# Kernel optimization log

Measured on AMD Instinct MI355X. Metric: run time of the kernel, lower is better.

Reference implementation:

```python
import jax, jax.numpy as jnp
import numpy as np
import math

B, C, T0, Q0 = 2, 48, 250, 65
H = 192; KS = 4; HS = 1; NH = 4; E = 8; F = 65; DV = 12; HID2 = 384
EPS = 1e-5


def ln_clamp(x, g, b, axes, eps=EPS):
    # LayerNormalization4D / 4DCF: std = sqrt(clamp(var, eps))
    mu = x.mean(axis=axes, keepdims=True)
    var = x.var(axis=axes, keepdims=True)
    return (x - mu) / jnp.sqrt(jnp.maximum(var, eps)) * g + b


def torch_ln(x, g, b, eps=EPS):
    # torch.nn.LayerNorm over last dim: sqrt(var + eps)
    mu = x.mean(axis=-1, keepdims=True)
    var = x.var(axis=-1, keepdims=True)
    return (x - mu) / jnp.sqrt(var + eps) * g + b


def mha(x, in_w, in_b, out_w, out_b, nh):
    # torch.nn.MultiheadAttention, batch_first, self-attention
    N, L, Cm = x.shape
    qkv = x @ in_w.T + in_b
    q, k, v = jnp.split(qkv, 3, axis=-1)
    dh = Cm // nh
    hd = lambda t: t.reshape(N, L, nh, dh).transpose(0, 2, 1, 3)
    q, k, v = hd(q), hd(k), hd(v)
    att = jax.nn.softmax(jnp.einsum('nhld,nhmd->nhlm', q, k) / jnp.sqrt(jnp.float32(dh)), axis=-1)
    o = jnp.einsum('nhlm,nhmd->nhld', att, v).transpose(0, 2, 1, 3).reshape(N, L, Cm)
    return o @ out_w.T + out_b


def lstm_dir(x, wi, wh, bi, bh, reverse=False):
    # x: [N, L, D]; torch gate order i,f,g,o
    Hd = wh.shape[1]
    xs = jnp.swapaxes(x, 0, 1)
    if reverse:
        xs = xs[::-1]
    pre = jnp.einsum('lnd,gd->lng', xs, wi) + bi + bh  # [L,N,4H]

    def step(carry, p):
        hprev, cprev = carry
        gates = p + hprev @ wh.T
        i, f, g, o = jnp.split(gates, 4, axis=-1)
        c = jax.nn.sigmoid(f) * cprev + jax.nn.sigmoid(i) * jnp.tanh(g)
        hnew = jax.nn.sigmoid(o) * jnp.tanh(c)
        return (hnew, c), hnew

    h0 = jnp.zeros((x.shape[0], Hd), x.dtype)
    _, ys = jax.lax.scan(step, (h0, h0), pre)
    if reverse:
        ys = ys[::-1]
    return jnp.swapaxes(ys, 0, 1)


def bilstm(x, wif, whf, bif, bhf, wib, whb, bib, bhb):
    return jnp.concatenate([lstm_dir(x, wif, whf, bif, bhf, False),
                            lstm_dir(x, wib, whb, bib, bhb, True)], axis=-1)


def unfold1d(x, ks, hs):
    # x: [N, C, Q] -> [N, L, C*ks], channel-major like F.unfold
    N, Cc, Qq = x.shape
    L = (Qq - ks) // hs + 1
    cols = jnp.stack([x[:, :, k:k + (L - 1) * hs + 1:hs] for k in range(ks)], axis=-1)  # [N,C,L,ks]
    return cols.transpose(0, 2, 1, 3).reshape(N, L, Cc * ks)


def conv_transpose1d(x, w, b, stride):
    # x: [N, Cin, L], w: [Cin, Cout, ks] (torch ConvTranspose1d layout); overlap-add
    N, Ci, L = x.shape
    ks = w.shape[2]
    out_len = (L - 1) * stride + ks
    y = jnp.einsum('nil,iok->nolk', x, w)
    out = jnp.zeros((N, w.shape[1], out_len), x.dtype)
    for k in range(ks):
        out = out.at[:, :, k:k + (L - 1) * stride + 1:stride].add(y[..., k])
    return out + b[:, None]


def _forward(x, af_in_w, af_in_b, af_out_w, af_out_b, naf_g, naf_b, at_in_w, at_in_b, at_out_w, at_out_b, nat_g, nat_b, intra_ng, intra_nb, inter_ng, inter_nb, intra_wif, intra_whf, intra_bif, intra_bhf, intra_wib, intra_whb, intra_bib, intra_bhb, inter_wif, inter_whf, inter_bif, inter_bhf, inter_wib, inter_whb, inter_bib, inter_bhb, il_w, il_b, itl_w, itl_b, qw, qb, qa, qg, qbt, kw, kb, ka, kg, kbt, vw, vb, va, vg, vbt, pw, pb, pa, pg, pbt, fin_w, fin_b, fdw_w, fdw_b, fout_w, fout_b):
    Bb, Cc, old_T, old_Q = x.shape
    T = math.ceil((old_T - KS) / HS) * HS + KS
    Qd = math.ceil((old_Q - KS) / HS) * HS + KS
    x = jnp.pad(x, ((0, 0), (0, 0), (0, T - old_T), (0, Qd - old_Q)))
    input_ = x

    # ---- intra (frequency) path ----
    z = ln_clamp(input_, intra_ng[None, :, None, None], intra_nb[None, :, None, None], (1,))
    seq = z.transpose(0, 2, 3, 1).reshape(Bb * T, Qd, Cc)  # [B*T, Q, C]
    att = mha(seq, af_in_w, af_in_b, af_out_w, af_out_b, NH)
    seq = torch_ln(att + seq, naf_g, naf_b)
    u = unfold1d(seq.transpose(0, 2, 1), KS, HS)
    r = bilstm(u, intra_wif, intra_whf, intra_bif, intra_bhf, intra_wib, intra_whb, intra_bib, intra_bhb)
    r = conv_transpose1d(r.transpose(0, 2, 1), il_w, il_b, HS)  # [B*T, C, Qd]
    intra = r.reshape(Bb, T, Cc, Qd).transpose(0, 2, 1, 3) + input_
    input_ = intra

    # ---- inter (time) path ----
    z = ln_clamp(input_, inter_ng[None, :, None, None], inter_nb[None, :, None, None], (1,))
    seq = z.transpose(0, 3, 2, 1).reshape(Bb * Qd, T, Cc)  # [B*Q, T, C]
    att = mha(seq, at_in_w, at_in_b, at_out_w, at_out_b, NH)
    seq = torch_ln(att + seq, nat_g, nat_b)
    u = unfold1d(seq.transpose(0, 2, 1), KS, HS)
    r = bilstm(u, inter_wif, inter_whf, inter_bif, inter_bhf, inter_wib, inter_whb, inter_bib, inter_bhb)
    r = conv_transpose1d(r.transpose(0, 2, 1), itl_w, itl_b, HS)  # [B*Qd, C, T]
    inter = r.reshape(Bb, Qd, Cc, T).transpose(0, 2, 3, 1) + input_
    inter = inter[:, :, :old_T, :old_Q]

    # ---- custom per-head conv attention ----
    bt = inter  # [B, C, t, f]

    def head_proj(w, bias, a, g, beta):
        y = jnp.einsum('bctf,hec->hbetf', bt, w) + bias[:, None, :, None, None]
        y = jnp.where(y >= 0, y, a[:, None, None, None, None] * y)  # PReLU per head
        return ln_clamp(y, g[:, None, :, None, :], beta[:, None, :, None, :], (2, 4))

    Qh = head_proj(qw, qb, qa, qg, qbt)  # [h,B,E,t,f]
    Kh = head_proj(kw, kb, ka, kg, kbt)
    Vh = head_proj(vw, vb, va, vg, vbt)  # [h,B,dv,t,f]
    h_, _, E_, t_, f_ = Qh.shape
    dv = Vh.shape[2]
    Qf = Qh.transpose(0, 1, 3, 2, 4).reshape(h_, Bb, t_, E_ * f_)
    Kf = Kh.transpose(0, 1, 3, 2, 4).reshape(h_, Bb, t_, E_ * f_)
    Vf = Vh.transpose(0, 1, 3, 2, 4).reshape(h_, Bb, t_, dv * f_)
    attm = jax.nn.softmax(jnp.einsum('hbtd,hbsd->hbts', Qf, Kf) / jnp.sqrt(jnp.float32(E_ * f_)), axis=-1)
    Vo = jnp.einsum('hbts,hbsd->hbtd', attm, Vf).reshape(h_, Bb, t_, dv, f_)
    Vo = Vo.transpose(1, 0, 3, 2, 4).reshape(Bb, h_ * dv, t_, f_)  # head-major channel concat
    pj = jnp.einsum('bctf,oc->botf', Vo, pw) + pb[None, :, None, None]
    pj = jnp.where(pj >= 0, pj, pa * pj)
    pj = ln_clamp(pj, pg[None, :, None, :], pbt[None, :, None, :], (1, 3))
    out = pj + inter

    # ---- gated-dconv FFN ----
    pi = jnp.einsum('bctf,oc->botf', out, fin_w) + fin_b[None, :, None, None]
    dwc = jax.lax.conv_general_dilated(pi, fdw_w, (1, 1), ((1, 1), (1, 1)),
                                       dimension_numbers=('NCHW', 'OIHW', 'NCHW'),
                                       feature_group_count=fdw_w.shape[0]) + fdw_b[None, :, None, None]
    x1, x2 = jnp.split(dwc, 2, axis=1)
    ffn = jnp.einsum('bctf,oc->botf', jax.nn.gelu(x1, approximate=False) * x2, fout_w) + fout_b[None, :, None, None]
    return ffn + out


def setup_inputs() -> dict:
    key = jax.random.key(0)
    cnt = [0]

    def rn(shape, s=0.05):
        cnt[0] += 1
        return jax.random.normal(jax.random.fold_in(key, cnt[0]), shape, dtype=jnp.float32) * s

    z = lambda *s: jnp.zeros(s, jnp.float32)
    o = lambda *s: jnp.ones(s, jnp.float32)
    d = {}
    d['x'] = rn((B, C, T0, Q0), 1.0)
    for p in ['af', 'at']:
        d[p + '_in_w'] = rn((3 * C, C)); d[p + '_in_b'] = z(3 * C)
        d[p + '_out_w'] = rn((C, C)); d[p + '_out_b'] = z(C)
    d['naf_g'] = o(C); d['naf_b'] = z(C); d['nat_g'] = o(C); d['nat_b'] = z(C)
    d['intra_ng'] = o(C); d['intra_nb'] = z(C); d['inter_ng'] = o(C); d['inter_nb'] = z(C)
    for p in ['intra', 'inter']:
        for s in ['f', 'b']:
            d[p + '_wi' + s] = rn((4 * H, C * KS)); d[p + '_wh' + s] = rn((4 * H, H))
            d[p + '_bi' + s] = z(4 * H); d[p + '_bh' + s] = z(4 * H)
    d['il_w'] = rn((2 * H, C, KS)); d['il_b'] = z(C)
    d['itl_w'] = rn((2 * H, C, KS)); d['itl_b'] = z(C)
    for p, dim in [('q', E), ('k', E), ('v', DV)]:
        d[p + 'w'] = rn((NH, dim, C)); d[p + 'b'] = z(NH, dim)
        d[p + 'a'] = 0.25 * o(NH); d[p + 'g'] = o(NH, dim, F); d[p + 'bt'] = z(NH, dim, F)
    d['pw'] = rn((C, C)); d['pb'] = z(C); d['pa'] = 0.25 * o(1); d['pg'] = o(C, F); d['pbt'] = z(C, F)
    d['fin_w'] = rn((HID2, C)); d['fin_b'] = z(HID2)
    d['fdw_w'] = rn((HID2, 1, 3, 3)); d['fdw_b'] = z(HID2)
    d['fout_w'] = rn((C, HID2 // 2)); d['fout_b'] = z(C)
    return d


def reference(x, af_in_w, af_in_b, af_out_w, af_out_b, naf_g, naf_b, at_in_w, at_in_b, at_out_w, at_out_b, nat_g, nat_b, intra_ng, intra_nb, inter_ng, inter_nb, intra_wif, intra_whf, intra_bif, intra_bhf, intra_wib, intra_whb, intra_bib, intra_bhb, inter_wif, inter_whf, inter_bif, inter_bhf, inter_wib, inter_whb, inter_bib, inter_bhb, il_w, il_b, itl_w, itl_b, qw, qb, qa, qg, qbt, kw, kb, ka, kg, kbt, vw, vb, va, vg, vbt, pw, pb, pa, pg, pbt, fin_w, fin_b, fdw_w, fdw_b, fout_w, fout_b):
    return _forward(x, af_in_w, af_in_b, af_out_w, af_out_b, naf_g, naf_b, at_in_w, at_in_b, at_out_w, at_out_b, nat_g, nat_b, intra_ng, intra_nb, inter_ng, inter_nb, intra_wif, intra_whf, intra_bif, intra_bhf, intra_wib, intra_whb, intra_bib, intra_bhb, inter_wif, inter_whf, inter_bif, inter_bhf, inter_wib, inter_whb, inter_bib, inter_bhb, il_w, il_b, itl_w, itl_b, qw, qb, qa, qg, qbt, kw, kb, ka, kg, kbt, vw, vb, va, vg, vbt, pw, pb, pa, pg, pbt, fin_w, fin_b, fdw_w, fdw_b, fout_w, fout_b)
```

## Files before the change

### kernel.cpp

```cpp
#include <hip/hip_runtime.h>
#include <math.h>

#define EPSV 1e-5f

typedef _Float16 v2h __attribute__((ext_vector_type(2)));

__device__ __forceinline__ float sigf(float x){ return 1.0f/(1.0f+__expf(-x)); }
__device__ __forceinline__ float tanhf_(float x){
  float c = fminf(fmaxf(x,-10.f),10.f);
  float e = __expf(2.0f*c);
  return (e-1.0f)/(e+1.0f);
}

__device__ __forceinline__ void ldsbar(){
  asm volatile("s_waitcnt lgkmcnt(0)\n\ts_barrier" ::: "memory");
}

__device__ __forceinline__ float dot2u(unsigned int a, unsigned int b, float c){
#if __has_builtin(__builtin_amdgcn_fdot2)
  v2h av = __builtin_bit_cast(v2h, a);
  v2h bv = __builtin_bit_cast(v2h, b);
  return __builtin_amdgcn_fdot2(av, bv, c, false);
#else
  v2h av = __builtin_bit_cast(v2h, a);
  v2h bv = __builtin_bit_cast(v2h, b);
  return c + (float)av.x*(float)bv.x + (float)av.y*(float)bv.y;
#endif
}

__global__ void k_ln_chan(const float* __restrict__ src, float* __restrict__ dst,
                          const float* __restrict__ g, const float* __restrict__ bb, int mode){
  int i = blockIdx.x*blockDim.x + threadIdx.x;
  const int total = 2*250*65;
  if (i >= total) return;
  int q = i % 65; int t = (i/65) % 250; int b = i/(65*250);
  const float* p = src + (size_t)b*48*250*65 + (size_t)t*65 + q;
  float s=0.f, ss=0.f;
  for (int c=0;c<48;c++){ float v = p[(size_t)c*250*65]; s+=v; ss+=v*v; }
  float mu = s*(1.0f/48.0f);
  float var = ss*(1.0f/48.0f) - mu*mu;
  float rs = rsqrtf(fmaxf(var, EPSV));
  float* d = (mode==0) ? dst + ((size_t)(b*250+t)*65 + q)*48
                       : dst + ((size_t)(b*65+q)*250 + t)*48;
  for (int c=0;c<48;c++){ float v = p[(size_t)c*250*65]; d[c] = (v-mu)*rs*g[c] + bb[c]; }
}

__global__ void k_qkv(const float* __restrict__ seq, const float* __restrict__ w,
                      const float* __restrict__ bias, float* __restrict__ qkv, int NL){
  int i = blockIdx.x*blockDim.x + threadIdx.x;
  if (i >= NL*144) return;
  int j = i % 144; int nl = i / 144;
  const float* srow = seq + (size_t)nl*48;
  const float* wrow = w + j*48;
  float acc = bias[j];
  for (int c=0;c<48;c++) acc += srow[c]*wrow[c];
  qkv[i] = acc;
}

__global__ void k_mha(const float* __restrict__ qkv, float* __restrict__ att, int N, int L){
  __shared__ float shq[250*12];
  __shared__ float shk[250*12];
  __shared__ float shv[250*12];
  int n = blockIdx.x, h = blockIdx.y;
  const float* base = qkv + (size_t)n*L*144 + h*12;
  for (int i = threadIdx.x; i < L*12; i += blockDim.x){
    int l = i/12, d = i%12;
    shq[i] = base[(size_t)l*144 + d];
    shk[i] = base[(size_t)l*144 + 48 + d];
    shv[i] = base[(size_t)l*144 + 96 + d];
  }
  __syncthreads();
  const float scale = 0.28867513459481287f;
  for (int r = threadIdx.x; r < L; r += blockDim.x){
    float m = -1e30f, den = 0.0f, o[12];
    for (int d=0; d<12; d++) o[d]=0.0f;
    const float* qr = shq + r*12;
    for (int j=0; j<L; j++){
      const float* kr = shk + j*12;
      float s = 0.f;
      for (int d=0; d<12; d++) s += qr[d]*kr[d];
      s *= scale;
      if (s > m){
        float corr = __expf(m - s);
        den *= corr;
        for (int d=0; d<12; d++) o[d] *= corr;
        m = s;
      }
      float e = __expf(s - m);
      den += e;
      const float* vr = shv + j*12;
      for (int d=0; d<12; d++) o[d] += e*vr[d];
    }
    float inv = 1.0f/den;
    float* outp = att + ((size_t)n*L + r)*48 + h*12;
    for (int d=0; d<12; d++) outp[d] = o[d]*inv;
  }
}

__global__ void k_projres(const float* __restrict__ att, const float* __restrict__ seq,
                          const float* __restrict__ w, const float* __restrict__ bias,
                          float* __restrict__ dst, int NL){
  int i = blockIdx.x*blockDim.x + threadIdx.x;
  if (i >= NL*48) return;
  int o = i % 48; int nl = i/48;
  const float* ar = att + (size_t)nl*48;
  const float* wr = w + o*48;
  float acc = bias[o] + seq[i];
  for (int c=0;c<48;c++) acc += ar[c]*wr[c];
  dst[i] = acc;
}

__global__ void k_rowln(float* __restrict__ buf, const float* __restrict__ g,
                        const float* __restrict__ bb, int NL){
  int nl = blockIdx.x*blockDim.x + threadIdx.x;
  if (nl >= NL) return;
  float* p = buf + (size_t)nl*48;
  float s=0.f, ss=0.f;
  for (int c=0;c<48;c++){ float v=p[c]; s+=v; ss+=v*v; }
  float mu = s*(1.0f/48.0f);
  float var = ss*(1.0f/48.0f) - mu*mu;
  float rs = rsqrtf(var + EPSV);
  for (int c=0;c<48;c++) p[c] = (p[c]-mu)*rs*g[c] + bb[c];
}

__global__ void k_prep(const float* __restrict__ s0, const float* __restrict__ s1,
                       const float* __restrict__ s2, const float* __restrict__ s3,
                       const float* __restrict__ s4, const float* __restrict__ s5,
                       const float* __restrict__ s6, const float* __restrict__ s7,
                       const float* __restrict__ c0, const float* __restrict__ c1,
                       unsigned int* __restrict__ wpk, unsigned int* __restrict__ wtp){
  int i = blockIdx.x*blockDim.x + threadIdx.x;
  if (i < 589824){
    int seg = i/73728, off = i - seg*73728;
    const float* w = (seg==0)?s0:(seg==1)?s1:(seg==2)?s2:(seg==3)?s3:(seg==4)?s4:(seg==5)?s5:(seg==6)?s6:s7;
    int g = off % 768, d2 = off / 768;
    v2h v; v.x = (_Float16)w[g*192 + 2*d2]; v.y = (_Float16)w[g*192 + 2*d2 + 1];
    wpk[(size_t)seg*73728 + (size_t)d2*768 + g] = __builtin_bit_cast(unsigned int, v);
  } else if (i < 589824 + 2*36864){
    int j = i - 589824;
    int seg = j/36864, off = j - seg*36864;
    const float* w = seg ? c1 : c0;
    int c = off % 48; int ii2 = (off/48) % 192; int k = off/(48*192);
    v2h v;
    v.x = (_Float16)w[(2*ii2)*192 + c*4 + k];
    v.y = (_Float16)w[(2*ii2+1)*192 + c*4 + k];
    wtp[(size_t)seg*36864 + off] = __builtin_bit_cast(unsigned int, v);
  }
}

__global__ __launch_bounds__(256) void k_pregates(
    const float* __restrict__ seq2, const unsigned int* __restrict__ wi,
    const float* __restrict__ bi, const float* __restrict__ bh,
    _Float16* __restrict__ pre, int L2, int SL){
  __shared__ unsigned int ut[96*16];
  int n = blockIdx.y;
  int l0 = blockIdx.x*16;
  int t = threadIdx.x;
  for (int idx=t; idx<1536; idx+=256){
    int l = idx & 15, d2 = idx >> 4;
    int li = l0 + l;
    int c = d2 >> 1, k0 = (d2 & 1)*2;
    float u0=0.f, u1=0.f;
    if (li < L2){
      const float* p = seq2 + ((size_t)n*SL + li)*48;
      u0 = p[k0*48 + c];
      u1 = p[(k0+1)*48 + c];
    }
    v2h v; v.x=(_Float16)u0; v.y=(_Float16)u1;
    ut[d2*16 + l] = __builtin_bit_cast(unsigned int, v);
  }
  __syncthreads();
  float acc[3][16];
  float b0 = bi[t] + bh[t];
  float b1 = bi[t+256] + bh[t+256];
  float b2 = bi[t+512] + bh[t+512];
  #pragma unroll
  for (int l=0;l<16;l++){ acc[0][l]=b0; acc[1][l]=b1; acc[2][l]=b2; }
  #pragma unroll 4
  for (int d2=0; d2<96; d2++){
    unsigned int w0 = wi[(size_t)d2*768 + t];
    unsigned int w1 = wi[(size_t)d2*768 + t + 256];
    unsigned int w2 = wi[(size_t)d2*768 + t + 512];
    const uint4* u4 = (const uint4*)(ut + d2*16);
    #pragma unroll
    for (int l4=0; l4<4; l4++){
      uint4 uu = u4[l4];
      acc[0][l4*4+0] = dot2u(uu.x, w0, acc[0][l4*4+0]);
      acc[0][l4*4+1] = dot2u(uu.y, w0, acc[0][l4*4+1]);
      acc[0][l4*4+2] = dot2u(uu.z, w0, acc[0][l4*4+2]);
      acc[0][l4*4+3] = dot2u(uu.w, w0, acc[0][l4*4+3]);
      acc[1][l4*4+0] = dot2u(uu.x, w1, acc[1][l4*4+0]);
      acc[1][l4*4+1] = dot2u(uu.y, w1, acc[1][l4*4+1]);
      acc[1][l4*4+2] = dot2u(uu.z, w1, acc[1][l4*4+2]);
      acc[1][l4*4+3] = dot2u(uu.w, w1, acc[1][l4*4+3]);
      acc[2][l4*4+0] = dot2u(uu.x, w2, acc[2][l4*4+0]);
      acc[2][l4*4+1] = dot2u(uu.y, w2, acc[2][l4*4+1]);
      acc[2][l4*4+2] = dot2u(uu.z, w2, acc[2][l4*4+2]);
      acc[2][l4*4+3] = dot2u(uu.w, w2, acc[2][l4*4+3]);
    }
  }
  #pragma unroll
  for (int l=0;l<16;l++){
    int li = l0 + l;
    if (li < L2){
      _Float16* pr = pre + ((size_t)n*L2 + li)*768;
      pr[t]       = (_Float16)acc[0][l];
      pr[t+256]   = (_Float16)acc[1][l];
      pr[t+512]   = (_Float16)acc[2][l];
    }
  }
}

template<int G>
__global__ __launch_bounds__(1024) void k_lstm6(
    const _Float16* __restrict__ pre, unsigned int* __restrict__ rT2,
    const unsigned int* __restrict__ wh_f, const unsigned int* __restrict__ wh_b,
    int N, int L2){
  __shared__ unsigned int hh2[96*G];
  __shared__ float gpart[4*G*768];
  _Float16* hh2h = (_Float16*)hh2;
  int t = threadIdx.x;
  int q = t >> 8, tt = t & 255;
  int dir = blockIdx.y;
  int n0 = blockIdx.x*G;
  const unsigned int* wh = dir ? wh_b : wh_f;
  unsigned int wq[24][3];
  #pragma unroll
  for (int i=0;i<24;i++){
    const unsigned int* wr = wh + (size_t)(q*24+i)*768 + tt;
    wq[i][0] = wr[0]; wq[i][1] = wr[256]; wq[i][2] = wr[512];
  }
  const _Float16* prd = pre + (size_t)dir*(size_t)N*L2*768;
  float cst = 0.f;
  int as = t/192, aj = t - as*192;
  bool actv = (t < 192*G);
  const unsigned short* pbase = (const unsigned short*)prd;
  if (actv) pbase = (const unsigned short*)(prd + ((size_t)(n0+as)*L2)*768) + aj;
  for (int idx=t; idx<96*G; idx+=1024) hh2[idx]=0u;
  __syncthreads();

  unsigned short c0=0,c1=0,c2=0,c3=0;
  {
    int l0 = dir ? (L2-1) : 0;
    if (actv){
      const unsigned short* pp = pbase + (size_t)l0*768;
      c0 = pp[0]; c1 = pp[192]; c2 = pp[384]; c3 = pp[576];
    }
  }

  for (int step=0; step<L2; step++){
    int l = dir ? (L2-1-step) : step;
    int stepn = (step+1 < L2) ? (step+1) : step;
    int ln = dir ? (L2-1-stepn) : stepn;
    unsigned short pn0=0,pn1=0,pn2=0,pn3=0;
    if (actv){
      const unsigned short* pp = pbase + (size_t)ln*768;
      pn0 = pp[0]; pn1 = pp[192]; pn2 = pp[384]; pn3 = pp[576];
    }

    float acc0[G], acc1[G], acc2[G];
    #pragma unroll
    for (int s=0;s<G;s++){ acc0[s]=0.f; acc1[s]=0.f; acc2[s]=0.f; }
    #pragma unroll
    for (int i=0;i<24;i++){
      unsigned int hhv[G];
      if (G==4){
        uint4 hv = ((const uint4*)hh2)[q*24+i];
        hhv[0]=hv.x; hhv[1]=hv.y; hhv[2]=hv.z; hhv[3]=hv.w;
      } else if (G==2){
        uint2 hv = ((const uint2*)hh2)[q*24+i];
        hhv[0]=hv.x; hhv[1]=hv.y;
      } else {
        hhv[0] = hh2[q*24+i];
      }
      unsigned int w0 = wq[i][0], w1 = wq[i][1], w2 = wq[i][2];
      #pragma unroll
      for (int s=0;s<G;s++){
        acc0[s] = dot2u(hhv[s], w0, acc0[s]);
        acc1[s] = dot2u(hhv[s], w1, acc1[s]);
        acc2[s] = dot2u(hhv[s], w2, acc2[s]);
      }
    }
    #pragma unroll
    for (int s=0;s<G;s++){
      gpart[(q*G+s)*768 + tt]       = acc0[s];
      gpart[(q*G+s)*768 + tt + 256] = acc1[s];
      gpart[(q*G+s)*768 + tt + 512] = acc2[s];
    }
    ldsbar();

    if (actv){
      float gi = (float)__builtin_bit_cast(_Float16, c0);
      float gf = (float)__builtin_bit_cast(_Float16, c1);
      float gg = (float)__builtin_bit_cast(_Float16, c2);
      float go = (float)__builtin_bit_cast(_Float16, c3);
      #pragma unroll
      for (int qq=0; qq<4; qq++){
        const float* gp = gpart + (qq*G+as)*768;
        gi += gp[aj]; gf += gp[aj+192]; gg += gp[aj+384]; go += gp[aj+576];
      }
      float ig = sigf(gi), fg = sigf(gf), g2 = tanhf_(gg), og = sigf(go);
      cst = fg*cst + ig*g2;
      float hn = og*tanhf_(cst);
      hh2h[((aj>>1)*G + as)*2 + (aj&1)] = (_Float16)hn;
    }
    ldsbar();

    if (t < 96*G){
      int s = t/96, ii2 = t - s*96;
      unsigned int v = hh2[ii2*G + s];
      rT2[((size_t)(n0+s)*192 + dir*96 + ii2)*L2 + l] = v;
    }
    c0 = pn0; c1 = pn1; c2 = pn2; c3 = pn3;
  }
}

__global__ __launch_bounds__(256) void k_convt4(
    const unsigned int* __restrict__ rT2, const unsigned int* __restrict__ wtp,
    const float* __restrict__ bias, const float* __restrict__ resid,
    float* __restrict__ dst, int L2, int OL, int mode){
  int n = blockIdx.y;
  int pos = blockIdx.x*64 + (threadIdx.x & 63);
  int cq = __builtin_amdgcn_readfirstlane((int)(threadIdx.x >> 6));
  float acc[12];
  #pragma unroll
  for (int c=0;c<12;c++) acc[c]=0.f;
  const unsigned int* rbase = rT2 + (size_t)n*192*L2;
  for (int k=0;k<4;k++){
    int l = pos - k;
    bool v = (l>=0) && (l<L2);
    int lc = v ? l : 0;
    const unsigned int* wk = wtp + (size_t)k*192*48 + cq*12;
    #pragma unroll 4
    for (int ii2=0; ii2<192; ii2++){
      unsigned int rp = v ? rbase[(size_t)ii2*L2 + lc] : 0u;
      const unsigned int* wrow = wk + ii2*48;
      #pragma unroll
      for (int c=0;c<12;c++) acc[c] = dot2u(rp, wrow[c], acc[c]);
    }
  }
  if (pos < OL){
    for (int c12=0;c12<12;c12++){
      int c = cq*12 + c12;
      size_t oidx;
      if (mode==0){ int b=n/250, t=n%250; oidx = (((size_t)b*48+c)*250+t)*65+pos; }
      else        { int b=n/65,  qq=n%65; oidx = (((size_t)b*48+c)*250+pos)*65+qq; }
      dst[oidx] = acc[c12] + bias[c] + resid[oidx];
    }
  }
}

__global__ __launch_bounds__(256) void k_hproj(
    const float* __restrict__ bt, const float* __restrict__ w,
    const float* __restrict__ bias, const float* __restrict__ alpha,
    const float* __restrict__ g, const float* __restrict__ beta,
    float* __restrict__ dst, int dim, int kt_mode){
  __shared__ float ybuf[780];
  __shared__ float r1[256];
  __shared__ float r2[256];
  int bx = blockIdx.x;
  int h = bx/500; int rem = bx - h*500; int b = rem/250; int t = rem - b*250;
  int ny = dim*65;
  int tid = threadIdx.x;
  const float* bbase = bt + (size_t)b*48*250*65 + (size_t)t*65;
  float al = alpha[h];
  float s=0.f, ss=0.f;
  for (int kidx=tid; kidx<ny; kidx+=256){
    int e = kidx/65, f = kidx - e*65;
    const float* wr = w + (h*dim+e)*48;
    float acc = bias[h*dim+e];
    for (int c=0;c<48;c++) acc += bbase[(size_t)c*250*65 + f]*wr[c];
    if (acc < 0.f) acc *= al;
    ybuf[kidx] = acc; s += acc; ss += acc*acc;
  }
  r1[tid]=s; r2[tid]=ss; __syncthreads();
  for (int st=128; st>0; st>>=1){
    if (tid<st){ r1[tid]+=r1[tid+st]; r2[tid]+=r2[tid+st]; }
    __syncthreads();
  }
  float mu = r1[0]/(float)ny, var = r2[0]/(float)ny - mu*mu;
  float rs = rsqrtf(fmaxf(var, EPSV));
  for (int kidx=tid; kidx<ny; kidx+=256){
    float y = (ybuf[kidx]-mu)*rs*g[h*ny+kidx] + beta[h*ny+kidx];
    if (kt_mode) dst[((size_t)(h*2+b)*520 + kidx)*250 + t] = y;
    else         dst[(size_t)bx*ny + kidx] = y;
  }
}

__global__ __launch_bounds__(256) void k_headattn2(
    const float* __restrict__ Qp, const float* __restrict__ KT,
    const float* __restrict__ Vp, float* __restrict__ Vo){
  __shared__ float qsh[10*520];
  __shared__ float psh[10*250];
  __shared__ float rinv[10];
  int t0 = blockIdx.x*10;
  int hb = blockIdx.y;
  int h = hb >> 1, b = hb & 1;
  int tid = threadIdx.x;
  const float* qbase = Qp + ((size_t)hb*250 + t0)*520;
  for (int i=tid; i<5200; i+=256) qsh[i] = qbase[i];
  __syncthreads();
  const float scale = 0.04385290096535147f;
  if (tid < 250){
    float sc[10];
    #pragma unroll
    for (int i=0;i<10;i++) sc[i]=0.f;
    const float* kcol = KT + (size_t)hb*520*250 + tid;
    for (int d=0; d<520; d++){
      float kv = kcol[(size_t)d*250];
      #pragma unroll
      for (int i=0;i<10;i++) sc[i] += qsh[i*520+d]*kv;
    }
    #pragma unroll
    for (int i=0;i<10;i++) psh[i*250+tid] = sc[i]*scale;
  }
  __syncthreads();
  if (tid < 10){
    float m = -1e30f;
    for (int s2=0;s2<250;s2++) m = fmaxf(m, psh[tid*250+s2]);
    float den = 0.f;
    for (int s2=0;s2<250;s2++){
      float e = __expf(psh[tid*250+s2]-m);
      psh[tid*250+s2]=e; den+=e;
    }
    rinv[tid] = 1.0f/den;
  }
  __syncthreads();
  float acc[10][4];
  #pragma unroll
  for (int i=0;i<10;i++)
    #pragma unroll
    for (int s=0;s<4;s++) acc[i][s]=0.f;
  for (int s2=0; s2<250; s2++){
    const float* vrow = Vp + ((size_t)hb*250 + s2)*780;
    float p[10];
    #pragma unroll
    for (int i=0;i<10;i++) p[i] = psh[i*250+s2];
    #pragma unroll
    for (int slot=0; slot<4; slot++){
      int d = tid + slot*256;
      if (d < 780){
        float v = vrow[d];
        #pragma unroll
        for (int i=0;i<10;i++) acc[i][slot] += p[i]*v;
      }
    }
  }
  #pragma unroll
  for (int slot=0; slot<4; slot++){
    int d = tid + slot*256;
    if (d < 780){
      int e = d/65, f = d - e*65;
      #pragma unroll
      for (int i=0;i<10;i++){
        Vo[(((size_t)b*48 + h*12 + e)*250 + (t0+i))*65 + f] = acc[i][slot]*rinv[i];
      }
    }
  }
}

__global__ void k_pproj(const float* __restrict__ Vo, const float* __restrict__ pw,
                        const float* __restrict__ pb, const float* __restrict__ pa,
                        float* __restrict__ pj){
  int i = blockIdx.x*blockDim.x + threadIdx.x;
  if (i >= 2*48*250*65) return;
  int f = i % 65;
  int t = (i/65) % 250;
  int o = (i/(65*250)) % 48;
  int b = i/(65*250*48);
  const float* vp = Vo + (size_t)b*48*250*65 + (size_t)t*65 + f;
  const float* wr = pw + o*48;
  float acc = pb[o];
  for (int c=0;c<48;c++) acc += vp[(size_t)c*250*65]*wr[c];
  if (acc < 0.f) acc *= pa[0];
  pj[i] = acc;
}

__global__ void k_pln(const float* __restrict__ pj, const float* __restrict__ pg,
                      const float* __restrict__ pbt, const float* __restrict__ inter,
                      float* __restrict__ outb){
  __shared__ float r1[256];
  __shared__ float r2[256];
  int bx = blockIdx.x;
  int t = bx % 250, b = bx/250;
  const float* base = pj + (size_t)b*48*250*65 + (size_t)t*65;
  float s=0.f, ss=0.f;
  for (int k=threadIdx.x; k<3120; k+=256){
    int c = k/65, f = k%65;
    float v = base[(size_t)c*250*65 + f];
    s+=v; ss+=v*v;
  }
  r1[threadIdx.x]=s; r2[threadIdx.x]=ss; __syncthreads();
  for (int st=128; st>0; st>>=1){
    if (threadIdx.x<st){ r1[threadIdx.x]+=r1[threadIdx.x+st]; r2[threadIdx.x]+=r2[threadIdx.x+st]; }
    __syncthreads();
  }
  float mu = r1[0]*(1.0f/3120.0f), var = r2[0]*(1.0f/3120.0f) - mu*mu;
  float rs = rsqrtf(fmaxf(var, EPSV));
  for (int k=threadIdx.x; k<3120; k+=256){
    int c = k/65, f = k%65;
    size_t idx = (((size_t)b*48+c)*250 + t)*65 + f;
    float v = pj[idx];
    outb[idx] = (v-mu)*rs*pg[c*65+f] + pbt[c*65+f] + inter[idx];
  }
}

__global__ void k_fin2(const float* __restrict__ outb, const float* __restrict__ w,
                       const float* __restrict__ bias, float* __restrict__ pi){
  int i = blockIdx.x*blockDim.x + threadIdx.x;
  if (i >= 2*96*250*65) return;
  int f = i % 65;
  int t = (i/65) % 250;
  int og = (i/(65*250)) % 96;
  int b = i/(65*250*96);
  const float* xp = outb + (size_t)b*48*250*65 + (size_t)t*65 + f;
  const float* w0 = w + og*4*48;
  float a0=bias[og*4], a1=bias[og*4+1], a2=bias[og*4+2], a3=bias[og*4+3];
  for (int c=0;c<48;c++){
    float xv = xp[(size_t)c*250*65];
    a0 += xv*w0[c]; a1 += xv*w0[48+c]; a2 += xv*w0[96+c]; a3 += xv*w0[144+c];
  }
  size_t o0 = (((size_t)b*384 + og*4)*250 + t)*65 + f;
  pi[o0] = a0; pi[o0+16250] = a1; pi[o0+2*16250] = a2; pi[o0+3*16250] = a3;
}

__global__ void k_dwg(const float* __restrict__ pi, const float* __restrict__ dw,
                      const float* __restrict__ db, float* __restrict__ gbuf){
  int i = blockIdx.x*blockDim.x + threadIdx.x;
  if (i >= 2*192*250*65) return;
  int f = i % 65;
  int t = (i/65) % 250;
  int j = (i/(65*250)) % 192;
  int b = i/(65*250*192);
  float x12[2];
  for (int half=0; half<2; half++){
    int ch = j + half*192;
    const float* base = pi + ((size_t)b*384 + ch)*250*65;
    const float* wr = dw + ch*9;
    float acc = db[ch];
    for (int dt=-1; dt<=1; dt++){
      int tt = t+dt;
      if (tt<0||tt>=250) continue;
      for (int df=-1; df<=1; df++){
        int ff = f+df;
        if (ff<0||ff>=65) continue;
        acc += base[(size_t)tt*65+ff]*wr[(dt+1)*3 + (df+1)];
      }
    }
    x12[half]=acc;
  }
  float x1 = x12[0];
  float g = 0.5f*x1*(1.0f+erff(x1*0.70710678118654752f));
  gbuf[i] = g * x12[1];
}

__global__ void k_final2(const float* __restrict__ gbuf, const float* __restrict__ w,
                         const float* __restrict__ bias, const float* __restrict__ outb,
                         float* __restrict__ dout){
  int i = blockIdx.x*blockDim.x + threadIdx.x;
  if (i >= 2*12*250*65) return;
  int f = i % 65;
  int t = (i/65) % 250;
  int og = (i/(65*250)) % 12;
  int b = i/(65*250*12);
  const float* gp = gbuf + (size_t)b*192*250*65 + (size_t)t*65 + f;
  const float* w0 = w + og*4*192;
  float a0=bias[og*4], a1=bias[og*4+1], a2=bias[og*4+2], a3=bias[og*4+3];
  for (int j=0;j<192;j++){
    float gv = gp[(size_t)j*250*65];
    a0 += gv*w0[j]; a1 += gv*w0[192+j]; a2 += gv*w0[384+j]; a3 += gv*w0[576+j];
  }
  size_t o0 = (((size_t)b*48 + og*4)*250 + t)*65 + f;
  dout[o0]         = a0 + outb[o0];
  dout[o0+16250]   = a1 + outb[o0+16250];
  dout[o0+2*16250] = a2 + outb[o0+2*16250];
  dout[o0+3*16250] = a3 + outb[o0+3*16250];
}

extern "C" void kernel_launch(void* const* d_in, const int* in_sizes, int n_in,
                              void* d_out, int out_size, void* d_ws, size_t ws_size,
                              hipStream_t stream) {
  (void)in_sizes; (void)n_in; (void)out_size; (void)ws_size;
  auto in = [&](int i){ return (const float*)d_in[i]; };
  const float* x        = in(0);
  const float* af_in_w  = in(1);  const float* af_in_b  = in(2);
  const float* af_out_w = in(3);  const float* af_out_b = in(4);
  const float* at_in_w  = in(5);  const float* at_in_b  = in(6);
  const float* at_out_w = in(7);  const float* at_out_b = in(8);
  const float* naf_g = in(9),  *naf_b = in(10), *nat_g = in(11), *nat_b = in(12);
  const float* intra_ng = in(13), *intra_nb = in(14), *inter_ng = in(15), *inter_nb = in(16);
  const float* intra_wif = in(17), *intra_whf = in(18), *intra_bif = in(19), *intra_bhf = in(20);
  const float* intra_wib = in(21), *intra_whb = in(22), *intra_bib = in(23), *intra_bhb = in(24);
  const float* inter_wif = in(25), *inter_whf = in(26), *inter_bif = in(27), *inter_bhf = in(28);
  const float* inter_wib = in(29), *inter_whb = in(30), *inter_bib = in(31), *inter_bhb = in(32);
  const float* il_w = in(33), *il_b = in(34), *itl_w = in(35), *itl_b = in(36);
  const float* qw = in(37), *qb = in(38), *qa = in(39), *qg = in(40), *qbt = in(41);
  const float* kw = in(42), *kb = in(43), *ka = in(44), *kg = in(45), *kbt = in(46);
  const float* vw = in(47), *vb = in(48), *va = in(49), *vg = in(50), *vbt = in(51);
  const float* pw = in(52), *pb = in(53), *pa = in(54), *pg = in(55), *pbt = in(56);
  const float* fin_w = in(57), *fin_b = in(58), *fdw_w = in(59), *fdw_b = in(60);
  const float* fout_w = in(61), *fout_b = in(62);

  float* ws = (float*)d_ws;
  float* buf_intra = ws + 0;
  float* buf_bt    = ws + 1560000;
  float* buf_out   = ws + 3120000;
  unsigned int* wpk = (unsigned int*)(ws + 4680000);
  unsigned int* wtp = (unsigned int*)(ws + 5269824);
  float* scr       = ws + 5343552;
  float* s_seq2 = scr;
  float* s_seq  = scr + 1560000;
  float* s_qkv  = scr + 3120000;
  float* s_att  = scr + 7800000;
  _Float16* s_pre = (_Float16*)(scr + 1560000);
  unsigned int* s_rT2 = (unsigned int*)(scr + 26220480);
  float* s_Qh = scr;
  float* s_KT = scr + 1040000;
  float* s_Vh = scr + 2080000;
  float* s_Vo = scr + 3640000;
  float* s_pj = scr + 5200000;
  float* s_pi = scr;
  float* s_g  = scr + 12480000;

  const int thr = 256;
  auto cdiv = [](int a, int b){ return (a+b-1)/b; };

  k_prep<<<cdiv(663552,thr),thr,0,stream>>>(
      intra_wif, intra_whf, intra_wib, intra_whb,
      inter_wif, inter_whf, inter_wib, inter_whb,
      il_w, itl_w, wpk, wtp);

  k_ln_chan<<<cdiv(2*250*65,thr), thr, 0, stream>>>(x, s_seq, intra_ng, intra_nb, 0);
  k_qkv<<<cdiv(500*65*144,thr), thr, 0, stream>>>(s_seq, af_in_w, af_in_b, s_qkv, 500*65);
  k_mha<<<dim3(500,4), 256, 0, stream>>>(s_qkv, s_att, 500, 65);
  k_projres<<<cdiv(500*65*48,thr), thr, 0, stream>>>(s_att, s_seq, af_out_w, af_out_b, s_seq2, 500*65);
  k_rowln<<<cdiv(32500,thr), thr, 0, stream>>>(s_seq2, naf_g, naf_b, 32500);
  {
    const size_t dstr = (size_t)500*62*768;
    k_pregates<<<dim3(4,500), 256, 0, stream>>>(s_seq2, wpk+0*73728, intra_bif, intra_bhf, s_pre,        62, 65);
    k_pregates<<<dim3(4,500), 256, 0, stream>>>(s_seq2, wpk+2*73728, intra_bib, intra_bhb, s_pre + dstr, 62, 65);
  }
  k_lstm6<2><<<dim3(250,2), 1024, 0, stream>>>(s_pre, s_rT2, wpk+1*73728, wpk+3*73728, 500, 62);
  k_convt4<<<dim3(2,500), 256, 0, stream>>>(s_rT2, wtp+0*36864, il_b, x, buf_intra, 62, 65, 0);

  k_ln_chan<<<cdiv(2*250*65,thr),thr,0,stream>>>(buf_intra, s_seq, inter_ng, inter_nb, 1);
  k_qkv<<<cdiv(130*250*144,thr),thr,0,stream>>>(s_seq, at_in_w, at_in_b, s_qkv, 130*250);
  k_mha<<<dim3(130,4), 256, 0, stream>>>(s_qkv, s_att, 130, 250);
  k_projres<<<cdiv(130*250*48,thr),thr,0,stream>>>(s_att, s_seq, at_out_w, at_out_b, s_seq2, 130*250);
  k_rowln<<<cdiv(32500,thr),thr,0,stream>>>(s_seq2, nat_g, nat_b, 32500);
  {
    const size_t dstr = (size_t)130*247*768;
    k_pregates<<<dim3(16,130), 256, 0, stream>>>(s_seq2, wpk+4*73728, inter_bif, inter_bhf, s_pre,        247, 250);
    k_pregates<<<dim3(16,130), 256, 0, stream>>>(s_seq2, wpk+6*73728, inter_bib, inter_bhb, s_pre + dstr, 247, 250);
  }
  k_lstm6<1><<<dim3(130,2), 1024, 0, stream>>>(s_pre, s_rT2, wpk+5*73728, wpk+7*73728, 130, 247);
  k_convt4<<<dim3(4,130), 256, 0, stream>>>(s_rT2, wtp+1*36864, itl_b, buf_intra, buf_bt, 247, 250, 1);

  k_hproj<<<2000,256,0,stream>>>(buf_bt, qw, qb, qa, qg, qbt, s_Qh, 8, 0);
  k_hproj<<<2000,256,0,stream>>>(buf_bt, kw, kb, ka, kg, kbt, s_KT, 8, 1);
  k_hproj<<<2000,256,0,stream>>>(buf_bt, vw, vb, va, vg, vbt, s_Vh, 12, 0);
  k_headattn2<<<dim3(25,8), 256, 0, stream>>>(s_Qh, s_KT, s_Vh, s_Vo);
  k_pproj<<<cdiv(2*48*250*65,thr),thr,0,stream>>>(s_Vo, pw, pb, pa, s_pj);
  k_pln<<<500,256,0,stream>>>(s_pj, pg, pbt, buf_bt, buf_out);

  k_fin2<<<cdiv(2*96*250*65,thr),thr,0,stream>>>(buf_out, fin_w, fin_b, s_pi);
  k_dwg<<<cdiv(2*192*250*65,thr),thr,0,stream>>>(s_pi, fdw_w, fdw_b, s_g);
  k_final2<<<cdiv(2*12*250*65,thr),thr,0,stream>>>(s_g, fout_w, fout_b, buf_out, (float*)d_out);
}
```

Baseline: 2.577 ms.

## Restructure LSTM to one sequence per block, stage hproj input, fuse pproj+LN

The LSTM recurrence kernel now runs one sequence per 256-thread block. Each thread keeps its full 96-entry fp16-pair weight column in registers, so the four-way partial-sum reduction through shared memory goes away. This launches more, smaller blocks but puts heavy pressure on registers (288 weight registers per thread), which risks spills. The head projection kernel stages the 48x65 input slab into shared memory instead of re-reading global memory for every output. The P projection and its layer norm are fused into one kernel, which drops the intermediate global buffer and a launch.

```diff
diff --git a/kernel.cpp b/kernel.cpp
--- a/kernel.cpp
+++ b/kernel.cpp
@@ -211,107 +211,72 @@
   }
 }
 
-template<int G>
-__global__ __launch_bounds__(1024) void k_lstm6(
+__global__ __launch_bounds__(256,1) void k_lstm7(
     const _Float16* __restrict__ pre, unsigned int* __restrict__ rT2,
     const unsigned int* __restrict__ wh_f, const unsigned int* __restrict__ wh_b,
     int N, int L2){
-  __shared__ unsigned int hh2[96*G];
-  __shared__ float gpart[4*G*768];
+  __shared__ unsigned int hh2[96];
+  __shared__ float gsh[768];
   _Float16* hh2h = (_Float16*)hh2;
   int t = threadIdx.x;
-  int q = t >> 8, tt = t & 255;
   int dir = blockIdx.y;
-  int n0 = blockIdx.x*G;
+  int n = blockIdx.x;
   const unsigned int* wh = dir ? wh_b : wh_f;
-  unsigned int wq[24][3];
+  unsigned int w0[96], w1[96], w2[96];
   #pragma unroll
-  for (int i=0;i<24;i++){
-    const unsigned int* wr = wh + (size_t)(q*24+i)*768 + tt;
-    wq[i][0] = wr[0]; wq[i][1] = wr[256]; wq[i][2] = wr[512];
-  }
-  const _Float16* prd = pre + (size_t)dir*(size_t)N*L2*768;
+  for (int d2=0; d2<96; d2++){
+    const unsigned int* wr = wh + (size_t)d2*768 + t;
+    w0[d2] = wr[0]; w1[d2] = wr[256]; w2[d2] = wr[512];
+  }
+  const _Float16* prd = pre + ((size_t)dir*N + (size_t)n)*(size_t)L2*768;
+  const unsigned short* pbase = (const unsigned short*)prd + t;
   float cst = 0.f;
-  int as = t/192, aj = t - as*192;
-  bool actv = (t < 192*G);
-  const unsigned short* pbase = (const unsigned short*)prd;
-  if (actv) pbase = (const unsigned short*)(prd + ((size_t)(n0+as)*L2)*768) + aj;
-  for (int idx=t; idx<96*G; idx+=1024) hh2[idx]=0u;
+  if (t < 96) hh2[t] = 0u;
   __syncthreads();
 
   unsigned short c0=0,c1=0,c2=0,c3=0;
   {
     int l0 = dir ? (L2-1) : 0;
-    if (actv){
+    if (t < 192){
       const unsigned short* pp = pbase + (size_t)l0*768;
-      c0 = pp[0]; c1 = pp[192]; c2 = pp[384]; c3 = pp[576];
+      c0=pp[0]; c1=pp[192]; c2=pp[384]; c3=pp[576];
     }
   }
 
   for (int step=0; step<L2; step++){
     int l = dir ? (L2-1-step) : step;
-    int stepn = (step+1 < L2) ? (step+1) : step;
+    int stepn = (step+1<L2)? step+1 : step;
     int ln = dir ? (L2-1-stepn) : stepn;
     unsigned short pn0=0,pn1=0,pn2=0,pn3=0;
-    if (actv){
+    if (t<192){
       const unsigned short* pp = pbase + (size_t)ln*768;
-      pn0 = pp[0]; pn1 = pp[192]; pn2 = pp[384]; pn3 = pp[576];
-    }
-
-    float acc0[G], acc1[G], acc2[G];
+      pn0=pp[0]; pn1=pp[192]; pn2=pp[384]; pn3=pp[576];
+    }
+    float a0=0.f, a1=0.f, a2=0.f;
     #pragma unroll
-    for (int s=0;s<G;s++){ acc0[s]=0.f; acc1[s]=0.f; acc2[s]=0.f; }
-    #pragma unroll
-    for (int i=0;i<24;i++){
-      unsigned int hhv[G];
-      if (G==4){
-        uint4 hv = ((const uint4*)hh2)[q*24+i];
-        hhv[0]=hv.x; hhv[1]=hv.y; hhv[2]=hv.z; hhv[3]=hv.w;
-      } else if (G==2){
-        uint2 hv = ((const uint2*)hh2)[q*24+i];
-        hhv[0]=hv.x; hhv[1]=hv.y;
-      } else {
-        hhv[0] = hh2[q*24+i];
-      }
-      unsigned int w0 = wq[i][0], w1 = wq[i][1], w2 = wq[i][2];
-      #pragma unroll
-      for (int s=0;s<G;s++){
-        acc0[s] = dot2u(hhv[s], w0, acc0[s]);
-        acc1[s] = dot2u(hhv[s], w1, acc1[s]);
-        acc2[s] = dot2u(hhv[s], w2, acc2[s]);
-      }
-    }
-    #pragma unroll
-    for (int s=0;s<G;s++){
-      gpart[(q*G+s)*768 + tt]       = acc0[s];
-      gpart[(q*G+s)*768 + tt + 256] = acc1[s];
-      gpart[(q*G+s)*768 + tt + 512] = acc2[s];
-    }
+    for (int d2=0; d2<96; d2++){
+      unsigned int h2 = hh2[d2];
+      a0 = dot2u(h2, w0[d2], a0);
+      a1 = dot2u(h2, w1[d2], a1);
+      a2 = dot2u(h2, w2[d2], a2);
+    }
+    gsh[t] = a0; gsh[t+256] = a1; gsh[t+512] = a2;
     ldsbar();
-
-    if (actv){
-      float gi = (float)__builtin_bit_cast(_Float16, c0);
-      float gf = (float)__builtin_bit_cast(_Float16, c1);
-      float gg = (float)__builtin_bit_cast(_Float16, c2);
-      float go = (float)__builtin_bit_cast(_Float16, c3);
-      #pragma unroll
-      for (int qq=0; qq<4; qq++){
-        const float* gp = gpart + (qq*G+as)*768;
-        gi += gp[aj]; gf += gp[aj+192]; gg += gp[aj+384]; go += gp[aj+576];
-      }
-      float ig = sigf(gi), fg = sigf(gf), g2 = tanhf_(gg), og = sigf(go);
+    if (t<192){
+      float gi = (float)__builtin_bit_cast(_Float16,c0) + gsh[t];
+      float gf = (float)__builtin_bit_cast(_Float16,c1) + gsh[t+192];
+      float gg = (float)__builtin_bit_cast(_Float16,c2) + gsh[t+384];
+      float go = (float)__builtin_bit_cast(_Float16,c3) + gsh[t+576];
+      float ig=sigf(gi), fg=sigf(gf), g2=tanhf_(gg), og=sigf(go);
       cst = fg*cst + ig*g2;
       float hn = og*tanhf_(cst);
-      hh2h[((aj>>1)*G + as)*2 + (aj&1)] = (_Float16)hn;
+      hh2h[t] = (_Float16)hn;
     }
     ldsbar();
-
-    if (t < 96*G){
-      int s = t/96, ii2 = t - s*96;
-      unsigned int v = hh2[ii2*G + s];
-      rT2[((size_t)(n0+s)*192 + dir*96 + ii2)*L2 + l] = v;
-    }
-    c0 = pn0; c1 = pn1; c2 = pn2; c3 = pn3;
+    if (t<96){
+      rT2[((size_t)n*192 + dir*96 + t)*L2 + l] = hh2[t];
+    }
+    c0=pn0; c1=pn1; c2=pn2; c3=pn3;
   }
 }
 
@@ -355,6 +320,7 @@
     const float* __restrict__ bias, const float* __restrict__ alpha,
     const float* __restrict__ g, const float* __restrict__ beta,
     float* __restrict__ dst, int dim, int kt_mode){
+  __shared__ float tsh[3120];
   __shared__ float ybuf[780];
   __shared__ float r1[256];
   __shared__ float r2[256];
@@ -363,13 +329,18 @@
   int ny = dim*65;
   int tid = threadIdx.x;
   const float* bbase = bt + (size_t)b*48*250*65 + (size_t)t*65;
+  for (int kidx=tid; kidx<3120; kidx+=256){
+    int c = kidx/65, f = kidx - c*65;
+    tsh[kidx] = bbase[(size_t)c*250*65 + f];
+  }
+  __syncthreads();
   float al = alpha[h];
   float s=0.f, ss=0.f;
   for (int kidx=tid; kidx<ny; kidx+=256){
     int e = kidx/65, f = kidx - e*65;
     const float* wr = w + (h*dim+e)*48;
     float acc = bias[h*dim+e];
-    for (int c=0;c<48;c++) acc += bbase[(size_t)c*250*65 + f]*wr[c];
+    for (int c=0;c<48;c++) acc += tsh[c*65+f]*wr[c];
     if (acc < 0.f) acc *= al;
     ybuf[kidx] = acc; s += acc; ss += acc*acc;
   }
@@ -459,49 +430,45 @@
   }
 }
 
-__global__ void k_pproj(const float* __restrict__ Vo, const float* __restrict__ pw,
-                        const float* __restrict__ pb, const float* __restrict__ pa,
-                        float* __restrict__ pj){
-  int i = blockIdx.x*blockDim.x + threadIdx.x;
-  if (i >= 2*48*250*65) return;
-  int f = i % 65;
-  int t = (i/65) % 250;
-  int o = (i/(65*250)) % 48;
-  int b = i/(65*250*48);
-  const float* vp = Vo + (size_t)b*48*250*65 + (size_t)t*65 + f;
-  const float* wr = pw + o*48;
-  float acc = pb[o];
-  for (int c=0;c<48;c++) acc += vp[(size_t)c*250*65]*wr[c];
-  if (acc < 0.f) acc *= pa[0];
-  pj[i] = acc;
-}
-
-__global__ void k_pln(const float* __restrict__ pj, const float* __restrict__ pg,
-                      const float* __restrict__ pbt, const float* __restrict__ inter,
-                      float* __restrict__ outb){
+__global__ __launch_bounds__(256) void k_pprojln(
+    const float* __restrict__ Vo, const float* __restrict__ pw,
+    const float* __restrict__ pb, const float* __restrict__ pa,
+    const float* __restrict__ pg, const float* __restrict__ pbt,
+    const float* __restrict__ inter, float* __restrict__ outb){
+  __shared__ float vsh[3120];
+  __shared__ float ysh[3120];
   __shared__ float r1[256];
   __shared__ float r2[256];
   int bx = blockIdx.x;
   int t = bx % 250, b = bx/250;
-  const float* base = pj + (size_t)b*48*250*65 + (size_t)t*65;
+  int tid = threadIdx.x;
+  const float* vbase = Vo + (size_t)b*48*250*65 + (size_t)t*65;
+  for (int k=tid; k<3120; k+=256){
+    int c = k/65, f = k - c*65;
+    vsh[k] = vbase[(size_t)c*250*65 + f];
+  }
+  __syncthreads();
+  float pav = pa[0];
   float s=0.f, ss=0.f;
-  for (int k=threadIdx.x; k<3120; k+=256){
-    int c = k/65, f = k%65;
-    float v = base[(size_t)c*250*65 + f];
-    s+=v; ss+=v*v;
-  }
-  r1[threadIdx.x]=s; r2[threadIdx.x]=ss; __syncthreads();
+  for (int k=tid; k<3120; k+=256){
+    int o = k/65, f = k - o*65;
+    const float* wr = pw + o*48;
+    float acc = pb[o];
+    for (int c=0;c<48;c++) acc += vsh[c*65+f]*wr[c];
+    if (acc < 0.f) acc *= pav;
+    ysh[k] = acc; s += acc; ss += acc*acc;
+  }
+  r1[tid]=s; r2[tid]=ss; __syncthreads();
   for (int st=128; st>0; st>>=1){
-    if (threadIdx.x<st){ r1[threadIdx.x]+=r1[threadIdx.x+st]; r2[threadIdx.x]+=r2[threadIdx.x+st]; }
+    if (tid<st){ r1[tid]+=r1[tid+st]; r2[tid]+=r2[tid+st]; }
     __syncthreads();
   }
   float mu = r1[0]*(1.0f/3120.0f), var = r2[0]*(1.0f/3120.0f) - mu*mu;
   float rs = rsqrtf(fmaxf(var, EPSV));
-  for (int k=threadIdx.x; k<3120; k+=256){
-    int c = k/65, f = k%65;
+  for (int k=tid; k<3120; k+=256){
+    int c = k/65, f = k - c*65;
     size_t idx = (((size_t)b*48+c)*250 + t)*65 + f;
-    float v = pj[idx];
-    outb[idx] = (v-mu)*rs*pg[c*65+f] + pbt[c*65+f] + inter[idx];
+    outb[idx] = (ysh[k]-mu)*rs*pg[k] + pbt[k] + inter[idx];
   }
 }
 
@@ -618,7 +585,6 @@
   float* s_KT = scr + 1040000;
   float* s_Vh = scr + 2080000;
   float* s_Vo = scr + 3640000;
-  float* s_pj = scr + 5200000;
   float* s_pi = scr;
   float* s_g  = scr + 12480000;
 
@@ -640,7 +606,7 @@
     k_pregates<<<dim3(4,500), 256, 0, stream>>>(s_seq2, wpk+0*73728, intra_bif, intra_bhf, s_pre,        62, 65);
     k_pregates<<<dim3(4,500), 256, 0, stream>>>(s_seq2, wpk+2*73728, intra_bib, intra_bhb, s_pre + dstr, 62, 65);
   }
-  k_lstm6<2><<<dim3(250,2), 1024, 0, stream>>>(s_pre, s_rT2, wpk+1*73728, wpk+3*73728, 500, 62);
+  k_lstm7<<<dim3(500,2), 256, 0, stream>>>(s_pre, s_rT2, wpk+1*73728, wpk+3*73728, 500, 62);
   k_convt4<<<dim3(2,500), 256, 0, stream>>>(s_rT2, wtp+0*36864, il_b, x, buf_intra, 62, 65, 0);
 
   k_ln_chan<<<cdiv(2*250*65,thr),thr,0,stream>>>(buf_intra, s_seq, inter_ng, inter_nb, 1);
@@ -653,15 +619,14 @@
     k_pregates<<<dim3(16,130), 256, 0, stream>>>(s_seq2, wpk+4*73728, inter_bif, inter_bhf, s_pre,        247, 250);
     k_pregates<<<dim3(16,130), 256, 0, stream>>>(s_seq2, wpk+6*73728, inter_bib, inter_bhb, s_pre + dstr, 247, 250);
   }
-  k_lstm6<1><<<dim3(130,2), 1024, 0, stream>>>(s_pre, s_rT2, wpk+5*73728, wpk+7*73728, 130, 247);
+  k_lstm7<<<dim3(130,2), 256, 0, stream>>>(s_pre, s_rT2, wpk+5*73728, wpk+7*73728, 130, 247);
   k_convt4<<<dim3(4,130), 256, 0, stream>>>(s_rT2, wtp+1*36864, itl_b, buf_intra, buf_bt, 247, 250, 1);
 
   k_hproj<<<2000,256,0,stream>>>(buf_bt, qw, qb, qa, qg, qbt, s_Qh, 8, 0);
   k_hproj<<<2000,256,0,stream>>>(buf_bt, kw, kb, ka, kg, kbt, s_KT, 8, 1);
   k_hproj<<<2000,256,0,stream>>>(buf_bt, vw, vb, va, vg, vbt, s_Vh, 12, 0);
   k_headattn2<<<dim3(25,8), 256, 0, stream>>>(s_Qh, s_KT, s_Vh, s_Vo);
-  k_pproj<<<cdiv(2*48*250*65,thr),thr,0,stream>>>(s_Vo, pw, pb, pa, s_pj);
-  k_pln<<<500,256,0,stream>>>(s_pj, pg, pbt, buf_bt, buf_out);
+  k_pprojln<<<500,256,0,stream>>>(s_Vo, pw, pb, pa, pg, pbt, buf_bt, buf_out);
 
   k_fin2<<<cdiv(2*96*250*65,thr),thr,0,stream>>>(buf_out, fin_w, fin_b, s_pi);
   k_dwg<<<cdiv(2*192*250*65,thr),thr,0,stream>>>(s_pi, fdw_w, fdw_b, s_g);
```

New measurement: 3.306 ms. 1.28x slower.
